# Kernel optimization log

Measured on AMD Instinct MI355X. Metric: run time of the kernel, lower is better.

The kernel has to match this reference:

```python
import jax, jax.numpy as jnp
import numpy as np

D = 128      # memory_dim
L = 64       # segment_len
SCALE = 1.0 / np.sqrt(D)
LN_EPS = 1e-5


def _layernorm(x, g, b):
    mu = x.mean(-1, keepdims=True)
    var = ((x - mu) ** 2).mean(-1, keepdims=True)
    return (x - mu) * jax.lax.rsqrt(var + LN_EPS) * g + b


def setup_inputs() -> dict:
    key = jax.random.key(0)
    ks = jax.random.split(key, 8)
    B, T, Hd = 4, 4096, 2048
    w = 0.02  # init scale for weight matrices
    return {
        "H": jax.random.normal(ks[0], (B, T, Hd), jnp.float32),
        "M": jax.random.normal(ks[1], (B, D, D), jnp.float32),  # [B,K=128,D=128]
        "ln_g": jnp.ones((Hd,), jnp.float32),
        "ln_b": jnp.zeros((Hd,), jnp.float32),
        "W_eta_w": jax.random.normal(ks[2], (Hd,), jnp.float32) * w,
        "W_eta_b": jnp.full((1,), -5.0, jnp.float32),
        "sum_q": jax.random.normal(ks[3], (D,), jnp.float32),
        "sp_w": jax.random.normal(ks[4], (Hd, D), jnp.float32) * w,
        "sp_b": jnp.zeros((D,), jnp.float32),
        "eta_ch": jnp.ones((D,), jnp.float32),
        "temp": jnp.ones((1,), jnp.float32),
        "W_qkv": jax.random.normal(ks[5], (Hd, 3 * D), jnp.float32) * w,
    }


def reference(H, M, ln_g, ln_b, W_eta_w, W_eta_b, sum_q, sp_w, sp_b, eta_ch, temp, W_qkv):
    B, T, _ = H.shape
    K = M.shape[1]
    S = T // L  # T chosen divisible by segment_len (no-pad branch)

    Hn = _layernorm(H, ln_g, ln_b)                      # [B,T,Hd]

    # ---- write_memory ----
    H_mem = Hn @ sp_w + sp_b                            # [B,T,D]
    eta_tokens = jnp.einsum('bth,h->bt', Hn, W_eta_w) + W_eta_b  # [B,T]

    H_segs = H_mem.reshape(B, S, L, D)
    summary_scores = jnp.einsum('d,bsld->bsl', sum_q, H_segs) * SCALE
    summary_w = jax.nn.softmax(summary_scores, axis=-1)
    Z_seg = jnp.einsum('bsl,bsld->bsd', summary_w, H_segs)       # [B,S,D]

    eta_sig = jax.nn.sigmoid(eta_tokens)                          # [B,T]
    eta_seg = eta_sig.reshape(B, S, L).max(axis=-1)[..., None]    # [B,S,1]

    scores = jnp.einsum('bsd,bkd->bsk', Z_seg, M) * SCALE * jnp.exp(temp)
    A = jax.nn.softmax(scores, axis=-1)                           # [B,S,K]
    DeltaM = jnp.einsum('bsk,bsd->bkd', A, Z_seg * eta_seg)       # [B,K,D]

    eta_avg = eta_seg.mean(axis=1, keepdims=True)                 # [B,1,1]
    gate = eta_avg * jax.nn.sigmoid(eta_ch)                       # [B,1,D]
    M_new = (1.0 - gate) * M + DeltaM / S

    norm_sq = jnp.sum(DeltaM ** 2) / S
    # diversity loss on M_new
    Mn = M_new / jnp.maximum(jnp.linalg.norm(M_new, axis=-1, keepdims=True), 1e-12)
    sim = jnp.einsum('bkd,bjd->bkj', Mn, Mn) * (1.0 - jnp.eye(K, dtype=M.dtype))
    div_loss = jnp.mean(sim ** 2)
    loss = norm_sq * 0.01 + div_loss * 0.1

    # ---- read_memory (from updated memory; K<=1024 -> dense softmax path) ----
    Q_r = Hn @ W_qkv[:, 2 * D:]                                   # [B,T,D]
    r_scores = jnp.einsum('btd,bkd->btk', Q_r, M_new)
    A_r = jax.nn.softmax(r_scores * 2.0, axis=-1)
    C = jnp.einsum('btk,bkd->btd', A_r, M_new)                    # [B,T,D]

    return C, loss
```

## Files before the change

### kernel.cpp

```cpp
#include <hip/hip_runtime.h>
#include <hip/hip_bf16.h>
#include <math.h>

#define HD   2048
#define DD   128
#define TT   4096
#define BB   4
#define MT   (BB*TT)
#define LSEG 64
#define SSEG 64
#define NCOL 256
#define SCALE_D 0.088388347648318447f

typedef _Float16 half8 __attribute__((ext_vector_type(8)));
typedef _Float16 half4v __attribute__((ext_vector_type(4)));
typedef float    f32x4 __attribute__((ext_vector_type(4)));

__device__ __forceinline__ float sigmf(float x){ return 1.f/(1.f+__expf(-x)); }

__device__ __forceinline__ void glds16(const void* g, void* l) {
  __builtin_amdgcn_global_load_lds(
      (const __attribute__((address_space(1))) unsigned int*)g,
      (__attribute__((address_space(3))) unsigned int*)l, 16, 0, 0);
}

__global__ void k_pre(const float* __restrict__ ln_g, const float* __restrict__ ln_b,
                      const float* __restrict__ sp_w, const float* __restrict__ sp_b,
                      const float* __restrict__ W_qkv, const float* __restrict__ W_eta_w,
                      const float* __restrict__ W_eta_b,
                      _Float16* __restrict__ Bp, float* __restrict__ s_vec,
                      float* __restrict__ cb_vec, float* __restrict__ we2,
                      float* __restrict__ scal)
{
  __shared__ float red1[256], red2[256];
  int n = blockIdx.x, t = threadIdx.x;
  float sp = 0.f, cp = 0.f;
  if (n < NCOL) {
    for (int h = t; h < HD; h += 256) {
      float w = (n < DD) ? sp_w[(size_t)h*DD + n] : W_qkv[(size_t)h*384 + 256 + (n-DD)];
      float g = ln_g[h], b = ln_b[h];
      Bp[(size_t)n*HD + h] = (_Float16)(g*w);
      sp += g*w; cp += b*w;
    }
  } else {
    for (int h = t; h < HD; h += 256) {
      float w = W_eta_w[h];
      float g = ln_g[h], b = ln_b[h];
      we2[h] = g*w;
      sp += g*w; cp += b*w;
    }
  }
  red1[t] = sp; red2[t] = cp;
  __syncthreads();
  for (int o = 128; o > 0; o >>= 1) {
    if (t < o) { red1[t] += red1[t+o]; red2[t] += red2[t+o]; }
    __syncthreads();
  }
  if (t == 0) {
    if (n < NCOL) {
      s_vec[n]  = red1[0];
      cb_vec[n] = red2[0] + ((n < DD) ? sp_b[n] : 0.f);
    } else {
      scal[0] = red1[0];
      scal[1] = red2[0] + W_eta_b[0];
      scal[2] = 0.f; scal[3] = 0.f;
    }
  }
}

__launch_bounds__(512, 4)
__global__ void k01(const float* __restrict__ H, const _Float16* __restrict__ Bp,
                    const float* __restrict__ s_vec, const float* __restrict__ cb_vec,
                    const float* __restrict__ we2, const float* __restrict__ scal,
                    const float* __restrict__ sum_q, const float* __restrict__ Mmat,
                    const float* __restrict__ temp,
                    float* __restrict__ Q_r, float* __restrict__ Zeta,
                    float* __restrict__ A_seg, float* __restrict__ eta_seg)
{
  __shared__ __align__(16) char pool[66560];
  __shared__ float smu[64], srs[64], seta[64];
  __shared__ float sq_s[128], w64_s[64], Zs[128], red_s[4];
  __shared__ float eta_sh_s;
  _Float16* sA   = (_Float16*)pool;
  _Float16* sB   = (_Float16*)(pool + 8192);
  float*    we_s = (float*)(pool + 57344);
  float*    sHm  = (float*)pool;

  int tid = threadIdx.x;
  int seg = blockIdx.x;
  int b   = seg >> 6;
  int m0  = seg * 64;
  int w = tid >> 6, lane = tid & 63;
  int wr = w >> 2, wc = w & 3;
  int fcol = lane & 15, kq = lane >> 4;

  ((float4*)we_s)[tid] = ((const float4*)we2)[tid];
  if (tid < 128) sq_s[tid] = sum_q[tid];
  __syncthreads();

  int r_l = tid >> 3, s4 = tid & 7;
  const float* aptr = H + (size_t)(m0 + r_l)*HD + s4*4;
  int bn[2], bsl[2];
#pragma unroll
  for (int i = 0; i < 2; ++i) {
    int idx = i*512 + tid;
    bn[i]  = idx >> 2;
    bsl[i] = (idx & 3) ^ ((bn[i] >> 1) & 3);
  }

  f32x4 acc[2][4];
#pragma unroll
  for (int i = 0; i < 2; ++i)
#pragma unroll
    for (int j = 0; j < 4; ++j) acc[i][j] = (f32x4){0.f,0.f,0.f,0.f};
  float s1 = 0.f, s2 = 0.f, se = 0.f;

  float4 paE = *(const float4*)(aptr);
  __builtin_amdgcn_sched_barrier(0);
  glds16(Bp + (size_t)bn[0]*HD + bsl[0]*8, sB + (size_t)tid*8);
  glds16(Bp + (size_t)bn[1]*HD + bsl[1]*8, sB + (size_t)(512 + tid)*8);
  __builtin_amdgcn_sched_barrier(0);
  float4 paO = *(const float4*)(aptr + 32);
  __builtin_amdgcn_sched_barrier(0);
  glds16(Bp + (size_t)bn[0]*HD + 32 + bsl[0]*8, sB + 8192 + (size_t)tid*8);
  glds16(Bp + (size_t)bn[1]*HD + 32 + bsl[1]*8, sB + 8192 + (size_t)(512 + tid)*8);
  __builtin_amdgcn_sched_barrier(0);

  int cur3 = 0;

#define KSTEP(K0V, SAB, P, VMASM, APREF, BISSUE)                              \
  {                                                                           \
    _Float16* sAc = sA + (SAB)*2048;                                          \
    _Float16* sBc = sB + cur3*8192;                                           \
    const int k0 = (K0V);                                                     \
    {                                                                         \
      float v0 = P.x, v1 = P.y, v2 = P.z, v3 = P.w;                           \
      const float4 u = *(const float4*)(we_s + k0 + s4*4);                    \
      s1 += (v0+v1)+(v2+v3);                                                  \
      s2 += (v0*v0+v1*v1)+(v2*v2+v3*v3);                                      \
      se += (v0*u.x+v1*u.y)+(v2*u.z+v3*u.w);                                  \
      half4v h; h.x=(_Float16)v0; h.y=(_Float16)v1;                           \
                h.z=(_Float16)v2; h.w=(_Float16)v3;                           \
      *(half4v*)&sAc[r_l*32 + (((s4>>1)^((r_l>>1)&3))<<3) + ((s4&1)<<2)] = h; \
    }                                                                         \
    asm volatile(VMASM ::: "memory");                                         \
    __builtin_amdgcn_s_barrier();                                             \
    __builtin_amdgcn_sched_barrier(0);                                        \
    if (BISSUE) {                                                             \
      int wb3 = cur3 + 2; if (wb3 >= 3) wb3 -= 3;                             \
      _Float16* sBn = sB + wb3*8192;                                          \
      const _Float16* bsrc = Bp + (k0 + 64);                                  \
      glds16(bsrc + (size_t)bn[0]*HD + bsl[0]*8, sBn + (size_t)tid*8);        \
      glds16(bsrc + (size_t)bn[1]*HD + bsl[1]*8, sBn + (size_t)(512+tid)*8);  \
      __builtin_amdgcn_sched_barrier(0);                                      \
    }                                                                         \
    if (APREF) {                                                              \
      P = *(const float4*)(aptr + k0 + 64);                                   \
      __builtin_amdgcn_sched_barrier(0);                                      \
    }                                                                         \
    __builtin_amdgcn_s_setprio(1);                                            \
    {                                                                         \
      half8 af[2], bf[4];                                                     \
      _Pragma("unroll")                                                       \
      for (int rt = 0; rt < 2; ++rt) {                                        \
        int r = wr*32 + rt*16 + fcol;                                         \
        af[rt] = *(half8*)&sAc[r*32 + ((kq ^ ((r>>1)&3))<<3)];                \
      }                                                                       \
      _Pragma("unroll")                                                       \
      for (int ct = 0; ct < 4; ++ct) {                                        \
        int n = wc*64 + ct*16 + fcol;                                         \
        bf[ct] = *(half8*)&sBc[n*32 + ((kq ^ ((n>>1)&3))<<3)];                \
      }                                                                       \
      _Pragma("unroll")                                                       \
      for (int rt = 0; rt < 2; ++rt)                                          \
        _Pragma("unroll")                                                     \
        for (int ct = 0; ct < 4; ++ct)                                        \
          acc[rt][ct] = __builtin_amdgcn_mfma_f32_16x16x32_f16(af[rt], bf[ct], acc[rt][ct], 0,0,0); \
    }                                                                         \
    __builtin_amdgcn_s_setprio(0);                                            \
    cur3 += 1; if (cur3 >= 3) cur3 -= 3;                                      \
  }

#pragma unroll 1
  for (int kp = 0; kp < 31; ++kp) {
    int j0 = kp*64;
    KSTEP(j0,      0, paE, "s_waitcnt vmcnt(3) lgkmcnt(0)", 1, 1)
    KSTEP(j0 + 32, 1, paO, "s_waitcnt vmcnt(3) lgkmcnt(0)", 1, 1)
  }
  KSTEP(1984, 0, paE, "s_waitcnt vmcnt(3) lgkmcnt(0)", 0, 0)
  KSTEP(2016, 1, paO, "s_waitcnt vmcnt(0) lgkmcnt(0)", 0, 0)
#undef KSTEP

  s1 += __shfl_xor(s1, 1); s1 += __shfl_xor(s1, 2); s1 += __shfl_xor(s1, 4);
  s2 += __shfl_xor(s2, 1); s2 += __shfl_xor(s2, 2); s2 += __shfl_xor(s2, 4);
  se += __shfl_xor(se, 1); se += __shfl_xor(se, 2); se += __shfl_xor(se, 4);
  float scal0 = scal[0], scal1 = scal[1];
  if (s4 == 0) {
    float mu   = s1 * (1.f/HD);
    float var  = s2 * (1.f/HD) - mu*mu;
    float rstd = rsqrtf(var + 1e-5f);
    smu[r_l] = mu; srs[r_l] = rstd;
    seta[r_l] = rstd*(se - mu*scal0) + scal1;
  }
  __syncthreads();

#pragma unroll
  for (int ct = 0; ct < 4; ++ct) {
    int nl = wc*64 + ct*16 + fcol;
    float sn = s_vec[nl], cbn = cb_vec[nl];
#pragma unroll
    for (int rt = 0; rt < 2; ++rt)
#pragma unroll
      for (int r = 0; r < 4; ++r) {
        int m = wr*32 + rt*16 + kq*4 + r;
        sHm[m*260 + nl] = srs[m]*(acc[rt][ct][r] - smu[m]*sn) + cbn;
      }
  }
  __syncthreads();

#pragma unroll
  for (int j = 0; j < 4; ++j) {
    int idx = j*512 + tid;
    int row = idx >> 5, c4 = (idx & 31)*4;
    *(float4*)&Q_r[(size_t)(m0 + row)*DD + c4] = *(float4*)&sHm[row*260 + 128 + c4];
  }

  if (w == 0) {
    float sc = 0.f;
    const float4* hrow = (const float4*)&sHm[lane*260];
#pragma unroll
    for (int d4 = 0; d4 < 32; ++d4) {
      float4 hv = hrow[d4];
      float4 qv = *(const float4*)&sq_s[d4*4];
      sc += hv.x*qv.x + hv.y*qv.y + hv.z*qv.z + hv.w*qv.w;
    }
    sc *= SCALE_D;
    float mx = sc;
    for (int o = 32; o > 0; o >>= 1) mx = fmaxf(mx, __shfl_xor(mx, o));
    float e = __expf(sc - mx);
    float sm = e;
    for (int o = 32; o > 0; o >>= 1) sm += __shfl_xor(sm, o);
    w64_s[lane] = e / sm;
  } else if (w == 1) {
    float ev = seta[lane];
    for (int o = 32; o > 0; o >>= 1) ev = fmaxf(ev, __shfl_xor(ev, o));
    if (lane == 0) { float es = sigmf(ev); eta_sh_s = es; eta_seg[seg] = es; }
  }
  __syncthreads();

  if (tid < 128) {
    float z = 0.f;
    for (int l = 0; l < 64; ++l) z += w64_s[l]*sHm[l*260 + tid];
    Zs[tid] = z;
    Zeta[(size_t)seg*DD + tid] = z * eta_sh_s;
  }
  __syncthreads();

  float sc2 = 0.f;
  if (tid < 128) {
    const float4* mrow = (const float4*)(Mmat + ((size_t)b*DD + tid)*DD);
#pragma unroll
    for (int d4 = 0; d4 < 32; ++d4) {
      float4 mv = mrow[d4];
      sc2 += mv.x*Zs[d4*4] + mv.y*Zs[d4*4+1] + mv.z*Zs[d4*4+2] + mv.w*Zs[d4*4+3];
    }
    sc2 *= SCALE_D * __expf(temp[0]);
    float mx = sc2;
    for (int o = 32; o > 0; o >>= 1) mx = fmaxf(mx, __shfl_xor(mx, o));
    if (lane == 0) red_s[w] = mx;
  }
  __syncthreads();
  float ev2 = 0.f;
  if (tid < 128) {
    float mx = fmaxf(red_s[0], red_s[1]);
    ev2 = __expf(sc2 - mx);
    float sm = ev2;
    for (int o = 32; o > 0; o >>= 1) sm += __shfl_xor(sm, o);
    if (lane == 0) red_s[2 + w] = sm;
  }
  __syncthreads();
  if (tid < 128) {
    float smt = red_s[2] + red_s[3];
    A_seg[(size_t)seg*DD + tid] = ev2 / smt;
  }
}

__global__ void k2b(const float* __restrict__ A_seg, const float* __restrict__ Zeta,
                    const float* __restrict__ eta_seg, const float* __restrict__ Mmat,
                    const float* __restrict__ eta_ch,
                    float* __restrict__ M_new, float* __restrict__ rns_arr,
                    float* __restrict__ scal)
{
  __shared__ float As[64][33];
  __shared__ __align__(16) float Zsl[64*128];
  __shared__ float rowp[32][8];
  __shared__ float eta_av;
  __shared__ float redb[4];
  int tid = threadIdx.x;
  int b = blockIdx.x >> 2, kq = blockIdx.x & 3;
  for (int i = tid; i < 64*32; i += 256) {
    int s = i >> 5, j = i & 31;
    As[s][j] = A_seg[((size_t)b*SSEG + s)*DD + kq*32 + j];
  }
  const float4* z4 = (const float4*)(Zeta + (size_t)b*SSEG*DD);
  float4* zs4 = (float4*)Zsl;
  for (int i = tid; i < 64*32; i += 256) zs4[i] = z4[i];
  if (tid < 64) {
    float ev = eta_seg[(size_t)b*SSEG + tid];
    for (int o=32;o>0;o>>=1) ev += __shfl_xor(ev, o);
    if (tid == 0) eta_av = ev * (1.f/SSEG);
  }
  __syncthreads();
  int kl = tid & 31, dg = tid >> 5;
  int k = kq*32 + kl, d0 = dg*16;
  float dm[16];
#pragma unroll
  for (int j=0;j<16;j++) dm[j]=0.f;
  for (int s = 0; s < 64; ++s) {
    float a = As[s][kl];
    const float* zr = &Zsl[s*128 + d0];
#pragma unroll
    for (int j=0;j<16;j++) dm[j] += a * zr[j];
  }
  float nsq = 0.f;
#pragma unroll
  for (int j=0;j<16;j++) nsq += dm[j]*dm[j];
  float eav = eta_av;
  float mn[16];
  float ss = 0.f;
#pragma unroll
  for (int j=0;j<16;j++) {
    int d = d0 + j;
    float gate = eav * sigmf(eta_ch[d]);
    float v = (1.f - gate)*Mmat[((size_t)b*DD + k)*DD + d] + dm[j]*(1.f/SSEG);
    mn[j] = v; ss += v*v;
  }
#pragma unroll
  for (int j=0;j<16;j+=4) {
    float4 v4; v4.x=mn[j]; v4.y=mn[j+1]; v4.z=mn[j+2]; v4.w=mn[j+3];
    *(float4*)&M_new[((size_t)b*DD + k)*DD + d0 + j] = v4;
  }
  rowp[kl][dg] = ss;
  for (int o=1;o<64;o<<=1) nsq += __shfl_xor(nsq, o);
  if ((tid&63)==0) redb[tid>>6] = nsq;
  __syncthreads();
  if (tid == 0) atomicAdd(&scal[2], redb[0]+redb[1]+redb[2]+redb[3]);
  if (tid < 32) {
    float t2 = 0.f;
#pragma unroll
    for (int g=0; g<8; ++g) t2 += rowp[tid][g];
    float nrm = sqrtf(t2);
    rns_arr[(size_t)b*DD + kq*32 + tid] = 1.f / fmaxf(nrm, 1e-12f);
  }
}

__global__ void k2d(const float* __restrict__ M_new, const float* __restrict__ rns_arr,
                    float* __restrict__ scal)
{
  __shared__ float kr[4][128];
  __shared__ float redb[4];
  int tid = threadIdx.x;
  int b = blockIdx.x >> 5, kq = blockIdx.x & 31;
  for (int i = tid; i < 4*128; i += 256) {
    int ki = i >> 7, d = i & 127;
    kr[ki][d] = M_new[((size_t)b*DD + kq*4 + ki)*DD + d];
  }
  __syncthreads();
  int j = tid & 127, kh = tid >> 7;
  const float* mj = &M_new[((size_t)b*DD + j)*DD];
  float rj = rns_arr[(size_t)b*DD + j];
  float dv = 0.f;
#pragma unroll
  for (int ki2 = 0; ki2 < 2; ++ki2) {
    int kil = kh*2 + ki2;
    int kk = kq*4 + kil;
    float dot = 0.f;
    for (int d = 0; d < 128; d += 4) {
      float4 a = *(const float4*)(mj + d);
      dot += a.x*kr[kil][d] + a.y*kr[kil][d+1] + a.z*kr[kil][d+2] + a.w*kr[kil][d+3];
    }
    if (kk != j) {
      float sv = dot * rj * rns_arr[(size_t)b*DD + kk];
      dv += sv*sv;
    }
  }
  for (int o=1;o<64;o<<=1) dv += __shfl_xor(dv, o);
  if ((tid&63)==0) redb[tid>>6] = dv;
  __syncthreads();
  if (tid==0) atomicAdd(&scal[3], redb[0]+redb[1]+redb[2]+redb[3]);
}

__launch_bounds__(256, 1)
__global__ void k3(const float* __restrict__ Q_r, const float* __restrict__ M_new,
                   const float* __restrict__ scal, float* __restrict__ out)
{
  __shared__ __align__(16) _Float16 Mq[128*132];
  __shared__ __align__(16) _Float16 Mt[128*136];
  __shared__ __align__(16) _Float16 Ps[64*132];
  int tid = threadIdx.x;
  int b = blockIdx.x >> 6, tile = blockIdx.x & 63;
  int t0 = tile*64;
  if (blockIdx.x == 0 && tid == 0) {
    float loss = 0.01f*(scal[2]*(1.f/SSEG)) + 0.1f*(scal[3]*(1.f/(BB*DD*DD)));
    out[(size_t)MT*DD] = loss;
  }
  const float4* m4 = (const float4*)(M_new + (size_t)b*DD*DD);
#pragma unroll
  for (int it = 0; it < 4; ++it) {
    int sb = it*256 + tid;
    int rb = sb & 31, cb = sb >> 5;
    int r0 = rb*4, c0 = cb*4;
    float a[4][4];
#pragma unroll
    for (int j = 0; j < 4; ++j) {
      float4 v = m4[(size_t)(r0+j)*32 + cb];
      a[j][0]=v.x; a[j][1]=v.y; a[j][2]=v.z; a[j][3]=v.w;
    }
#pragma unroll
    for (int j = 0; j < 4; ++j) {
      half4v h; h.x=(_Float16)a[j][0]; h.y=(_Float16)a[j][1];
                h.z=(_Float16)a[j][2]; h.w=(_Float16)a[j][3];
      *(half4v*)&Mq[(r0+j)*132 + c0] = h;
    }
#pragma unroll
    for (int j2 = 0; j2 < 4; ++j2) {
      half4v h; h.x=(_Float16)a[0][j2]; h.y=(_Float16)a[1][j2];
                h.z=(_Float16)a[2][j2]; h.w=(_Float16)a[3][j2];
      *(half4v*)&Mt[(c0+j2)*136 + r0] = h;
    }
  }
  int w = tid >> 6, lane = tid & 63;
  int fcol = lane & 15, kq = lane >> 4;
  int tokA = t0 + w*16 + fcol;
  size_t qbase = ((size_t)b*TT + tokA)*DD;
  half8 af[4];
#pragma unroll
  for (int ks = 0; ks < 4; ++ks) {
    float4 q0 = *(const float4*)&Q_r[qbase + ks*32 + kq*8];
    float4 q1 = *(const float4*)&Q_r[qbase + ks*32 + kq*8 + 4];
    half8 h;
    h[0]=(_Float16)q0.x; h[1]=(_Float16)q0.y; h[2]=(_Float16)q0.z; h[3]=(_Float16)q0.w;
    h[4]=(_Float16)q1.x; h[5]=(_Float16)q1.y; h[6]=(_Float16)q1.z; h[7]=(_Float16)q1.w;
    af[ks] = h;
  }
  __syncthreads();
  f32x4 sacc[8];
#pragma unroll
  for (int nt = 0; nt < 8; ++nt) sacc[nt] = (f32x4){0.f,0.f,0.f,0.f};
#pragma unroll
  for (int nt = 0; nt < 8; ++nt)
#pragma unroll
    for (int ks = 0; ks < 4; ++ks) {
      half8 bf = *(half8*)&Mq[(nt*16 + fcol)*132 + ks*32 + kq*8];
      sacc[nt] = __builtin_amdgcn_mfma_f32_16x16x32_f16(af[ks], bf, sacc[nt], 0,0,0);
    }
#pragma unroll
  for (int nt = 0; nt < 8; ++nt)
#pragma unroll
    for (int r = 0; r < 4; ++r) sacc[nt][r] *= 2.f;
  float mx[4], sm[4];
#pragma unroll
  for (int r = 0; r < 4; ++r) {
    float m = sacc[0][r];
#pragma unroll
    for (int nt = 1; nt < 8; ++nt) m = fmaxf(m, sacc[nt][r]);
#pragma unroll
    for (int o = 1; o < 16; o <<= 1) m = fmaxf(m, __shfl_xor(m, o));
    mx[r] = m;
  }
#pragma unroll
  for (int r = 0; r < 4; ++r) sm[r] = 0.f;
#pragma unroll
  for (int nt = 0; nt < 8; ++nt)
#pragma unroll
    for (int r = 0; r < 4; ++r) {
      float e = __expf(sacc[nt][r] - mx[r]);
      sacc[nt][r] = e; sm[r] += e;
    }
#pragma unroll
  for (int r = 0; r < 4; ++r) {
    float s = sm[r];
#pragma unroll
    for (int o = 1; o < 16; o <<= 1) s += __shfl_xor(s, o);
    sm[r] = 1.f / s;
  }
#pragma unroll
  for (int nt = 0; nt < 8; ++nt)
#pragma unroll
    for (int r = 0; r < 4; ++r) {
      int tk = w*16 + kq*4 + r;
      Ps[tk*132 + nt*16 + fcol] = (_Float16)(sacc[nt][r]*sm[r]);
    }
  __syncthreads();
  half8 pf[4];
#pragma unroll
  for (int ks = 0; ks < 4; ++ks)
    pf[ks] = *(half8*)&Ps[(w*16 + fcol)*132 + ks*32 + kq*8];
  f32x4 cacc[8];
#pragma unroll
  for (int nt = 0; nt < 8; ++nt) cacc[nt] = (f32x4){0.f,0.f,0.f,0.f};
#pragma unroll
  for (int nt = 0; nt < 8; ++nt)
#pragma unroll
    for (int ks = 0; ks < 4; ++ks) {
      half8 bf = *(half8*)&Mt[(nt*16 + fcol)*136 + ks*32 + kq*8];
      cacc[nt] = __builtin_amdgcn_mfma_f32_16x16x32_f16(pf[ks], bf, cacc[nt], 0,0,0);
    }
#pragma unroll
  for (int nt = 0; nt < 8; ++nt)
#pragma unroll
    for (int r = 0; r < 4; ++r) {
      int tk = t0 + w*16 + kq*4 + r;
      out[((size_t)b*TT + tk)*DD + nt*16 + fcol] = cacc[nt][r];
    }
}

extern "C" void kernel_launch(void* const* d_in, const int* in_sizes, int n_in,
                              void* d_out, int out_size, void* d_ws, size_t ws_size,
                              hipStream_t stream)
{
  (void)in_sizes; (void)n_in; (void)out_size; (void)ws_size;
  const float* H       = (const float*)d_in[0];
  const float* Mmat    = (const float*)d_in[1];
  const float* ln_g    = (const float*)d_in[2];
  const float* ln_b    = (const float*)d_in[3];
  const float* W_eta_w = (const float*)d_in[4];
  const float* W_eta_b = (const float*)d_in[5];
  const float* sum_q   = (const float*)d_in[6];
  const float* sp_w    = (const float*)d_in[7];
  const float* sp_b    = (const float*)d_in[8];
  const float* eta_ch  = (const float*)d_in[9];
  const float* temp    = (const float*)d_in[10];
  const float* W_qkv   = (const float*)d_in[11];
  float* out           = (float*)d_out;

  char* wsb = (char*)d_ws;
  size_t off = 0;
  auto alloc = [&](size_t bytes) -> void* {
    void* p = wsb + off;
    off = (off + bytes + 255) & ~(size_t)255;
    return p;
  };
  _Float16* Bp   = (_Float16*)alloc((size_t)NCOL*HD*2);
  float* s_vec   = (float*)alloc(NCOL*4);
  float* cb_vec  = (float*)alloc(NCOL*4);
  float* we2     = (float*)alloc(HD*4);
  float* scal    = (float*)alloc(4*4);
  float* Q_r     = (float*)alloc((size_t)MT*DD*4);
  float* Zeta    = (float*)alloc((size_t)BB*SSEG*DD*4);
  float* A_seg   = (float*)alloc((size_t)BB*SSEG*DD*4);
  float* eta_seg = (float*)alloc((size_t)BB*SSEG*4);
  float* M_new   = (float*)alloc((size_t)BB*DD*DD*4);
  float* rns_arr = (float*)alloc((size_t)BB*DD*4);

  hipLaunchKernelGGL(k_pre, dim3(NCOL+1), dim3(256), 0, stream,
                     ln_g, ln_b, sp_w, sp_b, W_qkv, W_eta_w, W_eta_b,
                     Bp, s_vec, cb_vec, we2, scal);
  hipLaunchKernelGGL(k01, dim3(MT/64), dim3(512), 0, stream,
                     H, Bp, s_vec, cb_vec, we2, scal, sum_q, Mmat, temp,
                     Q_r, Zeta, A_seg, eta_seg);
  hipLaunchKernelGGL(k2b, dim3(16), dim3(256), 0, stream,
                     A_seg, Zeta, eta_seg, Mmat, eta_ch, M_new, rns_arr, scal);
  hipLaunchKernelGGL(k2d, dim3(128), dim3(256), 0, stream,
                     M_new, rns_arr, scal);
  hipLaunchKernelGGL(k3, dim3(256), dim3(256), 0, stream,
                     Q_r, M_new, scal, out);
}
```

Before: 107.8 us.

## Split fused GEMM into 32-row tiles and move segment reduction to new kernel

The main LayerNorm+projection GEMM kernel now processes 32-row tiles instead of 64-row segments. This doubles the grid to 512 blocks, and it uses a K-step of 64 with double-buffered B tiles and a new swizzle. The per-segment summary softmax, eta max and memory-score softmax move to a separate k_seg kernel that reads H_mem and per-token eta from global memory. The eta weight vector is held in LDS as fp16. The goal is better CU occupancy and load balance on the dominant GEMM. The cost is an extra launch, an extra 8 MB write and read of H_mem, and slightly reduced precision in the eta dot product.

New measurement: 95.75 us. 1.13x faster.

```diff
diff --git a/kernel.cpp b/kernel.cpp
--- a/kernel.cpp
+++ b/kernel.cpp
@@ -72,165 +72,187 @@
 __global__ void k01(const float* __restrict__ H, const _Float16* __restrict__ Bp,
                     const float* __restrict__ s_vec, const float* __restrict__ cb_vec,
                     const float* __restrict__ we2, const float* __restrict__ scal,
-                    const float* __restrict__ sum_q, const float* __restrict__ Mmat,
-                    const float* __restrict__ temp,
-                    float* __restrict__ Q_r, float* __restrict__ Zeta,
-                    float* __restrict__ A_seg, float* __restrict__ eta_seg)
-{
-  __shared__ __align__(16) char pool[66560];
-  __shared__ float smu[64], srs[64], seta[64];
-  __shared__ float sq_s[128], w64_s[64], Zs[128], red_s[4];
-  __shared__ float eta_sh_s;
-  _Float16* sA   = (_Float16*)pool;
-  _Float16* sB   = (_Float16*)(pool + 8192);
-  float*    we_s = (float*)(pool + 57344);
-  float*    sHm  = (float*)pool;
+                    float* __restrict__ HmG, float* __restrict__ Q_r,
+                    float* __restrict__ eta_tok)
+{
+  __shared__ __align__(16) char pool[73728];
+  __shared__ _Float16 we_h[HD];
+  __shared__ float smu[32], srs[32];
+  _Float16* sA  = (_Float16*)pool;
+  _Float16* sB  = (_Float16*)(pool + 8192);
+  float*    sHm = (float*)pool;
 
   int tid = threadIdx.x;
-  int seg = blockIdx.x;
-  int b   = seg >> 6;
-  int m0  = seg * 64;
+  int m0  = blockIdx.x * 32;
   int w = tid >> 6, lane = tid & 63;
-  int wr = w >> 2, wc = w & 3;
   int fcol = lane & 15, kq = lane >> 4;
 
-  ((float4*)we_s)[tid] = ((const float4*)we2)[tid];
-  if (tid < 128) sq_s[tid] = sum_q[tid];
-  __syncthreads();
-
-  int r_l = tid >> 3, s4 = tid & 7;
-  const float* aptr = H + (size_t)(m0 + r_l)*HD + s4*4;
-  int bn[2], bsl[2];
-#pragma unroll
-  for (int i = 0; i < 2; ++i) {
+  {
+    float4 v = ((const float4*)we2)[tid];
+    half4v h; h.x=(_Float16)v.x; h.y=(_Float16)v.y;
+              h.z=(_Float16)v.z; h.w=(_Float16)v.w;
+    *(half4v*)&we_h[tid*4] = h;
+  }
+  float scal0 = scal[0], scal1 = scal[1];
+  __syncthreads();
+
+  int r_l = tid >> 4, s16 = tid & 15;
+  const float* aptr = H + (size_t)(m0 + r_l)*HD + s16*4;
+  int bn[4], bsl[4];
+#pragma unroll
+  for (int i = 0; i < 4; ++i) {
     int idx = i*512 + tid;
-    bn[i]  = idx >> 2;
-    bsl[i] = (idx & 3) ^ ((bn[i] >> 1) & 3);
-  }
-
-  f32x4 acc[2][4];
+    bn[i]  = idx >> 3;
+    bsl[i] = (idx & 7) ^ (bn[i] & 7);
+  }
+
+  f32x4 acc[2][2];
 #pragma unroll
   for (int i = 0; i < 2; ++i)
 #pragma unroll
-    for (int j = 0; j < 4; ++j) acc[i][j] = (f32x4){0.f,0.f,0.f,0.f};
+    for (int j = 0; j < 2; ++j) acc[i][j] = (f32x4){0.f,0.f,0.f,0.f};
   float s1 = 0.f, s2 = 0.f, se = 0.f;
 
   float4 paE = *(const float4*)(aptr);
   __builtin_amdgcn_sched_barrier(0);
-  glds16(Bp + (size_t)bn[0]*HD + bsl[0]*8, sB + (size_t)tid*8);
-  glds16(Bp + (size_t)bn[1]*HD + bsl[1]*8, sB + (size_t)(512 + tid)*8);
+#pragma unroll
+  for (int i = 0; i < 4; ++i)
+    glds16(Bp + (size_t)bn[i]*HD + bsl[i]*8, sB + (size_t)(i*512 + tid)*8);
   __builtin_amdgcn_sched_barrier(0);
-  float4 paO = *(const float4*)(aptr + 32);
+  float4 paO = *(const float4*)(aptr + 64);
   __builtin_amdgcn_sched_barrier(0);
-  glds16(Bp + (size_t)bn[0]*HD + 32 + bsl[0]*8, sB + 8192 + (size_t)tid*8);
-  glds16(Bp + (size_t)bn[1]*HD + 32 + bsl[1]*8, sB + 8192 + (size_t)(512 + tid)*8);
-  __builtin_amdgcn_sched_barrier(0);
-
-  int cur3 = 0;
 
 #define KSTEP(K0V, SAB, P, VMASM, APREF, BISSUE)                              \
   {                                                                           \
     _Float16* sAc = sA + (SAB)*2048;                                          \
-    _Float16* sBc = sB + cur3*8192;                                           \
+    _Float16* sBc = sB + (SAB)*16384;                                         \
     const int k0 = (K0V);                                                     \
     {                                                                         \
       float v0 = P.x, v1 = P.y, v2 = P.z, v3 = P.w;                           \
-      const float4 u = *(const float4*)(we_s + k0 + s4*4);                    \
+      half4v uh = *(half4v*)&we_h[k0 + s16*4];                                \
+      float u0 = (float)uh.x, u1 = (float)uh.y,                               \
+            u2 = (float)uh.z, u3 = (float)uh.w;                               \
       s1 += (v0+v1)+(v2+v3);                                                  \
       s2 += (v0*v0+v1*v1)+(v2*v2+v3*v3);                                      \
-      se += (v0*u.x+v1*u.y)+(v2*u.z+v3*u.w);                                  \
+      se += (v0*u0+v1*u1)+(v2*u2+v3*u3);                                      \
       half4v h; h.x=(_Float16)v0; h.y=(_Float16)v1;                           \
                 h.z=(_Float16)v2; h.w=(_Float16)v3;                           \
-      *(half4v*)&sAc[r_l*32 + (((s4>>1)^((r_l>>1)&3))<<3) + ((s4&1)<<2)] = h; \
+      *(half4v*)&sAc[r_l*64 + (((s16>>1) ^ (r_l & 7))<<3) + ((s16&1)<<2)] = h;\
     }                                                                         \
     asm volatile(VMASM ::: "memory");                                         \
     __builtin_amdgcn_s_barrier();                                             \
     __builtin_amdgcn_sched_barrier(0);                                        \
     if (BISSUE) {                                                             \
-      int wb3 = cur3 + 2; if (wb3 >= 3) wb3 -= 3;                             \
-      _Float16* sBn = sB + wb3*8192;                                          \
+      _Float16* sBn = sB + ((SAB)^1)*16384;                                   \
       const _Float16* bsrc = Bp + (k0 + 64);                                  \
-      glds16(bsrc + (size_t)bn[0]*HD + bsl[0]*8, sBn + (size_t)tid*8);        \
-      glds16(bsrc + (size_t)bn[1]*HD + bsl[1]*8, sBn + (size_t)(512+tid)*8);  \
+      _Pragma("unroll")                                                       \
+      for (int i = 0; i < 4; ++i)                                             \
+        glds16(bsrc + (size_t)bn[i]*HD + bsl[i]*8,                            \
+               sBn + (size_t)(i*512 + tid)*8);                                \
       __builtin_amdgcn_sched_barrier(0);                                      \
     }                                                                         \
     if (APREF) {                                                              \
-      P = *(const float4*)(aptr + k0 + 64);                                   \
+      P = *(const float4*)(aptr + k0 + 128);                                  \
       __builtin_amdgcn_sched_barrier(0);                                      \
     }                                                                         \
     __builtin_amdgcn_s_setprio(1);                                            \
-    {                                                                         \
-      half8 af[2], bf[4];                                                     \
+    _Pragma("unroll")                                                         \
+    for (int ks = 0; ks < 2; ++ks) {                                          \
+      half8 af[2], bf[2];                                                     \
       _Pragma("unroll")                                                       \
       for (int rt = 0; rt < 2; ++rt) {                                        \
-        int r = wr*32 + rt*16 + fcol;                                         \
-        af[rt] = *(half8*)&sAc[r*32 + ((kq ^ ((r>>1)&3))<<3)];                \
+        int r = rt*16 + fcol;                                                 \
+        int ch = (ks*4 + kq) ^ (r & 7);                                       \
+        af[rt] = *(half8*)&sAc[r*64 + ch*8];                                  \
       }                                                                       \
       _Pragma("unroll")                                                       \
-      for (int ct = 0; ct < 4; ++ct) {                                        \
-        int n = wc*64 + ct*16 + fcol;                                         \
-        bf[ct] = *(half8*)&sBc[n*32 + ((kq ^ ((n>>1)&3))<<3)];                \
+      for (int ct = 0; ct < 2; ++ct) {                                        \
+        int n = w*32 + ct*16 + fcol;                                          \
+        int ch = (ks*4 + kq) ^ (n & 7);                                       \
+        bf[ct] = *(half8*)&sBc[n*64 + ch*8];                                  \
       }                                                                       \
       _Pragma("unroll")                                                       \
       for (int rt = 0; rt < 2; ++rt)                                          \
         _Pragma("unroll")                                                     \
-        for (int ct = 0; ct < 4; ++ct)                                        \
+        for (int ct = 0; ct < 2; ++ct)                                        \
           acc[rt][ct] = __builtin_amdgcn_mfma_f32_16x16x32_f16(af[rt], bf[ct], acc[rt][ct], 0,0,0); \
     }                                                                         \
     __builtin_amdgcn_s_setprio(0);                                            \
-    cur3 += 1; if (cur3 >= 3) cur3 -= 3;                                      \
   }
 
 #pragma unroll 1
-  for (int kp = 0; kp < 31; ++kp) {
-    int j0 = kp*64;
-    KSTEP(j0,      0, paE, "s_waitcnt vmcnt(3) lgkmcnt(0)", 1, 1)
-    KSTEP(j0 + 32, 1, paO, "s_waitcnt vmcnt(3) lgkmcnt(0)", 1, 1)
-  }
-  KSTEP(1984, 0, paE, "s_waitcnt vmcnt(3) lgkmcnt(0)", 0, 0)
-  KSTEP(2016, 1, paO, "s_waitcnt vmcnt(0) lgkmcnt(0)", 0, 0)
+  for (int kp = 0; kp < 15; ++kp) {
+    int j0 = kp*128;
+    KSTEP(j0,      0, paE, "s_waitcnt vmcnt(1) lgkmcnt(0)", 1, 1)
+    KSTEP(j0 + 64, 1, paO, "s_waitcnt vmcnt(1) lgkmcnt(0)", 1, 1)
+  }
+  KSTEP(1920, 0, paE, "s_waitcnt vmcnt(1) lgkmcnt(0)", 0, 1)
+  KSTEP(1984, 1, paO, "s_waitcnt vmcnt(0) lgkmcnt(0)", 0, 0)
 #undef KSTEP
 
-  s1 += __shfl_xor(s1, 1); s1 += __shfl_xor(s1, 2); s1 += __shfl_xor(s1, 4);
-  s2 += __shfl_xor(s2, 1); s2 += __shfl_xor(s2, 2); s2 += __shfl_xor(s2, 4);
-  se += __shfl_xor(se, 1); se += __shfl_xor(se, 2); se += __shfl_xor(se, 4);
-  float scal0 = scal[0], scal1 = scal[1];
-  if (s4 == 0) {
+  s1 += __shfl_xor(s1, 1); s1 += __shfl_xor(s1, 2);
+  s1 += __shfl_xor(s1, 4); s1 += __shfl_xor(s1, 8);
+  s2 += __shfl_xor(s2, 1); s2 += __shfl_xor(s2, 2);
+  s2 += __shfl_xor(s2, 4); s2 += __shfl_xor(s2, 8);
+  se += __shfl_xor(se, 1); se += __shfl_xor(se, 2);
+  se += __shfl_xor(se, 4); se += __shfl_xor(se, 8);
+  if (s16 == 0) {
     float mu   = s1 * (1.f/HD);
     float var  = s2 * (1.f/HD) - mu*mu;
     float rstd = rsqrtf(var + 1e-5f);
     smu[r_l] = mu; srs[r_l] = rstd;
-    seta[r_l] = rstd*(se - mu*scal0) + scal1;
-  }
-  __syncthreads();
-
-#pragma unroll
-  for (int ct = 0; ct < 4; ++ct) {
-    int nl = wc*64 + ct*16 + fcol;
+    eta_tok[m0 + r_l] = rstd*(se - mu*scal0) + scal1;
+  }
+  __syncthreads();
+
+#pragma unroll
+  for (int ct = 0; ct < 2; ++ct) {
+    int nl = w*32 + ct*16 + fcol;
     float sn = s_vec[nl], cbn = cb_vec[nl];
 #pragma unroll
     for (int rt = 0; rt < 2; ++rt)
 #pragma unroll
       for (int r = 0; r < 4; ++r) {
-        int m = wr*32 + rt*16 + kq*4 + r;
+        int m = rt*16 + kq*4 + r;
         sHm[m*260 + nl] = srs[m]*(acc[rt][ct][r] - smu[m]*sn) + cbn;
       }
   }
   __syncthreads();
 
 #pragma unroll
-  for (int j = 0; j < 4; ++j) {
+  for (int j = 0; j < 2; ++j) {
     int idx = j*512 + tid;
     int row = idx >> 5, c4 = (idx & 31)*4;
+    *(float4*)&HmG[(size_t)(m0 + row)*DD + c4] = *(float4*)&sHm[row*260 + c4];
     *(float4*)&Q_r[(size_t)(m0 + row)*DD + c4] = *(float4*)&sHm[row*260 + 128 + c4];
   }
-
+}
+
+__global__ void k_seg(const float* __restrict__ HmG, const float* __restrict__ eta_tok,
+                      const float* __restrict__ Mmat, const float* __restrict__ sum_q,
+                      const float* __restrict__ temp,
+                      float* __restrict__ Zeta, float* __restrict__ A_seg,
+                      float* __restrict__ eta_seg)
+{
+  __shared__ __align__(16) float Hs[64*132];
+  __shared__ float sq_s[128], w64_s[64], red_s[4], Zs[128];
+  __shared__ float eta_sh_s;
+  int tid = threadIdx.x;
+  int seg = blockIdx.x, b = seg >> 6;
+  const float4* src = (const float4*)(HmG + (size_t)seg*64*DD);
+  for (int i = tid; i < 2048; i += 128) {
+    int row = i >> 5, c4 = (i & 31)*4;
+    *(float4*)&Hs[row*132 + c4] = src[i];
+  }
+  sq_s[tid] = sum_q[tid];
+  __syncthreads();
+  int w = tid >> 6, lane = tid & 63;
   if (w == 0) {
     float sc = 0.f;
-    const float4* hrow = (const float4*)&sHm[lane*260];
+    const float* hrow = &Hs[lane*132];
 #pragma unroll
     for (int d4 = 0; d4 < 32; ++d4) {
-      float4 hv = hrow[d4];
+      float4 hv = *(const float4*)&hrow[d4*4];
       float4 qv = *(const float4*)&sq_s[d4*4];
       sc += hv.x*qv.x + hv.y*qv.y + hv.z*qv.z + hv.w*qv.w;
     }
@@ -241,48 +263,36 @@
     float sm = e;
     for (int o = 32; o > 0; o >>= 1) sm += __shfl_xor(sm, o);
     w64_s[lane] = e / sm;
-  } else if (w == 1) {
-    float ev = seta[lane];
+  } else {
+    float ev = eta_tok[(size_t)seg*64 + lane];
     for (int o = 32; o > 0; o >>= 1) ev = fmaxf(ev, __shfl_xor(ev, o));
     if (lane == 0) { float es = sigmf(ev); eta_sh_s = es; eta_seg[seg] = es; }
   }
   __syncthreads();
-
-  if (tid < 128) {
-    float z = 0.f;
-    for (int l = 0; l < 64; ++l) z += w64_s[l]*sHm[l*260 + tid];
-    Zs[tid] = z;
-    Zeta[(size_t)seg*DD + tid] = z * eta_sh_s;
-  }
-  __syncthreads();
-
+  float z = 0.f;
+  for (int l = 0; l < 64; ++l) z += w64_s[l]*Hs[l*132 + tid];
+  Zs[tid] = z;
+  Zeta[(size_t)seg*DD + tid] = z * eta_sh_s;
+  __syncthreads();
   float sc2 = 0.f;
-  if (tid < 128) {
-    const float4* mrow = (const float4*)(Mmat + ((size_t)b*DD + tid)*DD);
-#pragma unroll
-    for (int d4 = 0; d4 < 32; ++d4) {
-      float4 mv = mrow[d4];
-      sc2 += mv.x*Zs[d4*4] + mv.y*Zs[d4*4+1] + mv.z*Zs[d4*4+2] + mv.w*Zs[d4*4+3];
-    }
-    sc2 *= SCALE_D * __expf(temp[0]);
-    float mx = sc2;
-    for (int o = 32; o > 0; o >>= 1) mx = fmaxf(mx, __shfl_xor(mx, o));
-    if (lane == 0) red_s[w] = mx;
-  }
-  __syncthreads();
-  float ev2 = 0.f;
-  if (tid < 128) {
-    float mx = fmaxf(red_s[0], red_s[1]);
-    ev2 = __expf(sc2 - mx);
-    float sm = ev2;
-    for (int o = 32; o > 0; o >>= 1) sm += __shfl_xor(sm, o);
-    if (lane == 0) red_s[2 + w] = sm;
-  }
-  __syncthreads();
-  if (tid < 128) {
-    float smt = red_s[2] + red_s[3];
-    A_seg[(size_t)seg*DD + tid] = ev2 / smt;
-  }
+  const float4* mrow = (const float4*)(Mmat + ((size_t)b*DD + tid)*DD);
+#pragma unroll
+  for (int d4 = 0; d4 < 32; ++d4) {
+    float4 mv = mrow[d4];
+    sc2 += mv.x*Zs[d4*4] + mv.y*Zs[d4*4+1] + mv.z*Zs[d4*4+2] + mv.w*Zs[d4*4+3];
+  }
+  sc2 *= SCALE_D * __expf(temp[0]);
+  float mx2 = sc2;
+  for (int o = 32; o > 0; o >>= 1) mx2 = fmaxf(mx2, __shfl_xor(mx2, o));
+  if (lane == 0) red_s[w] = mx2;
+  __syncthreads();
+  float mxa = fmaxf(red_s[0], red_s[1]);
+  float ev2 = __expf(sc2 - mxa);
+  float sm2 = ev2;
+  for (int o = 32; o > 0; o >>= 1) sm2 += __shfl_xor(sm2, o);
+  if (lane == 0) red_s[2 + w] = sm2;
+  __syncthreads();
+  A_seg[(size_t)seg*DD + tid] = ev2 / (red_s[2] + red_s[3]);
 }
 
 __global__ void k2b(const float* __restrict__ A_seg, const float* __restrict__ Zeta,
@@ -547,6 +557,8 @@
   float* we2     = (float*)alloc(HD*4);
   float* scal    = (float*)alloc(4*4);
   float* Q_r     = (float*)alloc((size_t)MT*DD*4);
+  float* HmG     = (float*)alloc((size_t)MT*DD*4);
+  float* eta_tok = (float*)alloc((size_t)MT*4);
   float* Zeta    = (float*)alloc((size_t)BB*SSEG*DD*4);
   float* A_seg   = (float*)alloc((size_t)BB*SSEG*DD*4);
   float* eta_seg = (float*)alloc((size_t)BB*SSEG*4);
@@ -556,9 +568,11 @@
   hipLaunchKernelGGL(k_pre, dim3(NCOL+1), dim3(256), 0, stream,
                      ln_g, ln_b, sp_w, sp_b, W_qkv, W_eta_w, W_eta_b,
                      Bp, s_vec, cb_vec, we2, scal);
-  hipLaunchKernelGGL(k01, dim3(MT/64), dim3(512), 0, stream,
-                     H, Bp, s_vec, cb_vec, we2, scal, sum_q, Mmat, temp,
-                     Q_r, Zeta, A_seg, eta_seg);
+  hipLaunchKernelGGL(k01, dim3(MT/32), dim3(512), 0, stream,
+                     H, Bp, s_vec, cb_vec, we2, scal,
+                     HmG, Q_r, eta_tok);
+  hipLaunchKernelGGL(k_seg, dim3(BB*SSEG), dim3(128), 0, stream,
+                     HmG, eta_tok, Mmat, sum_q, temp, Zeta, A_seg, eta_seg);
   hipLaunchKernelGGL(k2b, dim3(16), dim3(256), 0, stream,
                      A_seg, Zeta, eta_seg, Mmat, eta_ch, M_new, rns_arr, scal);
   hipLaunchKernelGGL(k2d, dim3(128), dim3(256), 0, stream,
```
